# Kernel optimization log

Measured on AMD Instinct MI355X. Metric: run time of the kernel, lower is better.

The kernel has to match this reference:

```python
import jax, jax.numpy as jnp
import numpy as np

R = 32            # voxel resolution
DIM = 240         # channels C
EPS_NORM = 0.0    # module eps
BN_EPS = 1e-5     # torch BatchNorm1d default eps


def setup_inputs() -> dict:
    key = jax.random.key(0)
    k1, k2, k3 = jax.random.split(key, 3)
    B, C, N = 4, DIM, 32768
    features = jax.random.normal(k1, (B, C, N), jnp.float32)
    coords = jax.random.uniform(k2, (B, 3, N), jnp.float32)
    # mlp params: Conv1d(2C -> C, kernel 1) + BatchNorm1d(C)
    w = jax.random.normal(k3, (C, 2 * C), jnp.float32) / np.sqrt(2 * C).astype(np.float32)
    b = jnp.zeros((C,), jnp.float32)
    gamma = jnp.ones((C,), jnp.float32)
    beta = jnp.zeros((C,), jnp.float32)
    return {"features": features, "coords": coords, "w": w, "b": b, "gamma": gamma, "beta": beta}


def _voxelize(features, coords):
    # normalize coords into [0, 1], scale to voxel grid
    nc = coords - coords.mean(axis=2, keepdims=True)                      # [B,3,N]
    scale = jnp.linalg.norm(nc, axis=1, keepdims=True).max(axis=2, keepdims=True) * 2.0 + EPS_NORM
    nc = nc / scale + 0.5
    nc = jnp.clip(nc * R, 0, R - 1)
    vox = jnp.round(nc).astype(jnp.int32)
    pos = vox[:, 0] + vox[:, 1] * R + vox[:, 2] * (R * R)                 # [B,N] flattened voxel id
    R3 = R * R * R

    def per_batch(f, p):
        # f: [C,N], p: [N] -> [2C, R3]; per-voxel max feature + second (min) feature
        mx = jax.ops.segment_max(f.T, p, num_segments=R3)                 # [R3, C]
        mn = jax.ops.segment_min(f.T, p, num_segments=R3)                 # [R3, C]
        cnt = jax.ops.segment_sum(jnp.ones_like(p), p, num_segments=R3)  # [R3]
        mask = (cnt > 0)[:, None]
        mx = jnp.where(mask, mx, 0.0)
        mn = jnp.where(mask, mn, 0.0)
        return jnp.concatenate([mx, mn], axis=1).T                        # [2C, R3]

    fea = jax.vmap(per_batch)(features, pos)                              # [B,2C,R3]
    return fea, nc


def reference(features, coords, w, b, gamma, beta):
    fea, nc = _voxelize(features, coords)
    # 1x1 Conv1d (pointwise GEMM) + BatchNorm1d (training-mode batch stats) + Swish
    y = jnp.einsum('co,bov->bcv', w, fea) + b[None, :, None]
    mean = y.mean(axis=(0, 2), keepdims=True)
    var = y.var(axis=(0, 2), keepdims=True)
    y = gamma[None, :, None] * (y - mean) * jax.lax.rsqrt(var + BN_EPS) + beta[None, :, None]
    y = y * jax.nn.sigmoid(y)
    B, C, _ = features.shape
    return y.reshape(B, C, R, R, R), nc
```

## Files before the change

kernel.cpp:

```cpp
#include <hip/hip_runtime.h>
#include <cstdint>
#include <cstddef>

#define RR 32
#define R3 32768
#define NPT 32768
#define CH 240
#define CH2 480
#define NB 4
#define NTILES 2048
#define Y_ELEMS 31457280

typedef __attribute__((ext_vector_type(8))) short short8v;
typedef __attribute__((ext_vector_type(4))) short short4v;
typedef __attribute__((ext_vector_type(4))) float float4v;

union u8pack { short8v v; unsigned short u[8]; };
union u4pack { short4v v; unsigned short u[4]; };

static __device__ __forceinline__ float bf2f(unsigned short u) {
  return __uint_as_float(((unsigned int)u) << 16);
}
static __device__ __forceinline__ unsigned short f2bf(float f) {
  unsigned int u = __float_as_uint(f);
  u = (u + 0x7FFFu + ((u >> 16) & 1u)) >> 16;
  return (unsigned short)u;
}

__global__ void k_init(int* __restrict__ cnt, float* __restrict__ stats,
                       const float* __restrict__ w, unsigned short* __restrict__ wfrag,
                       int* __restrict__ tilectr) {
  int g = blockIdx.x * 256 + threadIdx.x;
  if (g == 0) *tilectr = 0;
  if (g < NB * R3) cnt[g] = 0;
  if (g < 4096) stats[g] = 0.0f;
  if (g < 14400) {
    int lane = g & 63, t = g >> 6;
    int mg = t / 75, r = t % 75;
    int kc = r / 5, mL = r % 5;
    int m = mg * 5 + mL;
    int ln = lane & 15, q = lane >> 4;
    const float* src = w + (size_t)(m * 16 + ln) * CH2 + kc * 32 + q * 8;
    u8pack pk;
#pragma unroll
    for (int j = 0; j < 8; j++) pk.u[j] = f2bf(src[j]);
    *(short8v*)&wfrag[(size_t)g * 8] = pk.v;
  }
}

__global__ __launch_bounds__(1024) void k_coord_stats(const float* __restrict__ coords,
                                                      float* __restrict__ ms) {
  __shared__ float red[1024];
  __shared__ float mean[3];
  int b = blockIdx.x, t = threadIdx.x;
  const float4* cb4 = (const float4*)(coords + (size_t)b * 3 * NPT);
  float s[3] = {0.f, 0.f, 0.f};
  for (int i = t; i < NPT / 4; i += 1024) {
#pragma unroll
    for (int d = 0; d < 3; d++) {
      float4 v = cb4[d * (NPT / 4) + i];
      s[d] += (v.x + v.y) + (v.z + v.w);
    }
  }
  for (int d = 0; d < 3; d++) {
    red[t] = s[d]; __syncthreads();
    for (int k = 512; k > 0; k >>= 1) { if (t < k) red[t] += red[t + k]; __syncthreads(); }
    if (t == 0) mean[d] = red[0] * (1.0f / NPT);
    __syncthreads();
  }
  float m0 = mean[0], m1 = mean[1], m2 = mean[2];
  float mx = 0.f;
  for (int i = t; i < NPT / 4; i += 1024) {
    float4 x = cb4[i], y = cb4[NPT / 4 + i], z = cb4[2 * (NPT / 4) + i];
    float dx, dy, dz, n;
    dx = x.x - m0; dy = y.x - m1; dz = z.x - m2; n = dx * dx + dy * dy + dz * dz; mx = fmaxf(mx, n);
    dx = x.y - m0; dy = y.y - m1; dz = z.y - m2; n = dx * dx + dy * dy + dz * dz; mx = fmaxf(mx, n);
    dx = x.z - m0; dy = y.z - m1; dz = z.z - m2; n = dx * dx + dy * dy + dz * dz; mx = fmaxf(mx, n);
    dx = x.w - m0; dy = y.w - m1; dz = z.w - m2; n = dx * dx + dy * dy + dz * dz; mx = fmaxf(mx, n);
  }
  red[t] = mx; __syncthreads();
  for (int k = 512; k > 0; k >>= 1) { if (t < k) red[t] = fmaxf(red[t], red[t + k]); __syncthreads(); }
  if (t == 0) {
    ms[b * 4 + 0] = m0; ms[b * 4 + 1] = m1; ms[b * 4 + 2] = m2;
    ms[b * 4 + 3] = sqrtf(red[0]) * 2.0f;
  }
}

__global__ void k_pos_nc(const float* __restrict__ coords, const float* __restrict__ ms,
                         float* __restrict__ ncout, int* __restrict__ pos, int* __restrict__ cnt) {
  int g = blockIdx.x * 256 + threadIdx.x;
  int b = g >> 15, i = g & (NPT - 1);
  const float* cb = coords + (size_t)b * 3 * NPT;
  float scale = ms[b * 4 + 3];
  int vox[3];
#pragma unroll
  for (int d = 0; d < 3; d++) {
    float v = (cb[(size_t)d * NPT + i] - ms[b * 4 + d]) / scale + 0.5f;
    v = fminf(fmaxf(v * (float)RR, 0.0f), (float)(RR - 1));
    ncout[((size_t)(b * 3 + d)) * NPT + i] = v;
    vox[d] = (int)rintf(v);
  }
  int p = (b << 15) | (vox[0] + (vox[1] << 5) + (vox[2] << 10));
  pos[g] = p;
  atomicAdd(&cnt[p], 1);
}

__global__ void k_scan(const int* __restrict__ cnt, int* __restrict__ offs) {
  __shared__ int part[1024];
  int b = blockIdx.x, t = threadIdx.x;
  const int base = b * R3;
  int local[32];
  int s = 0;
#pragma unroll
  for (int j = 0; j < 32; j++) { local[j] = cnt[base + t * 32 + j]; s += local[j]; }
  part[t] = s; __syncthreads();
  for (int d = 1; d < 1024; d <<= 1) {
    int v = (t >= d) ? part[t - d] : 0;
    __syncthreads();
    part[t] += v;
    __syncthreads();
  }
  int run = (t == 0) ? 0 : part[t - 1];
#pragma unroll
  for (int j = 0; j < 32; j++) { offs[base + t * 32 + j] = run; run += local[j]; }
}

__global__ void k_scatter(const int* __restrict__ pos, int* __restrict__ offs,
                          int* __restrict__ rank) {
  int g = blockIdx.x * 256 + threadIdx.x;
  int p = pos[g];
  int slot = atomicAdd(&offs[p], 1);
  rank[g] = slot;
}

__global__ __launch_bounds__(256, 4) void k_transpose3(const float* __restrict__ f,
                                                       const int* __restrict__ rank,
                                                       unsigned short* __restrict__ fts) {
  __shared__ unsigned short tile[CH * 68];
  __shared__ int slts[64];
  int p0 = blockIdx.x * 64, b = blockIdx.y;
  int t = threadIdx.x;
  if (t < 64) slts[t] = rank[b * NPT + p0 + t];
  {
    int pg = t & 15, cq = t >> 4;
    const float* src = f + ((size_t)b * CH + cq) * NPT + p0 + pg * 4;
#pragma unroll
    for (int j = 0; j < 15; ++j) {
      float4 v = *(const float4*)(src + (size_t)(j * 16) * NPT);
      int c = j * 16 + cq;
      u4pack p4;
      p4.u[0] = f2bf(v.x); p4.u[1] = f2bf(v.y); p4.u[2] = f2bf(v.z); p4.u[3] = f2bf(v.w);
      *(short4v*)&tile[c * 68 + pg * 4] = p4.v;
    }
  }
  __syncthreads();
  int ch8 = t & 7;
#pragma unroll
  for (int pass = 0; pass < 2; ++pass) {
    int p = pass * 32 + (t >> 3);
    unsigned short* dst = fts + ((size_t)(b * NPT + slts[p])) * CH;
#pragma unroll
    for (int i = 0; i < 4; ++i) {
      int ch = ch8 + 8 * i;
      if (ch < 30) {
        u8pack pk;
#pragma unroll
        for (int jj = 0; jj < 8; ++jj) pk.u[jj] = tile[(ch * 8 + jj) * 68 + p];
        *(short8v*)&dst[ch * 8] = pk.v;
      }
    }
  }
}

__global__ __launch_bounds__(512, 2) void k_fused(const int* __restrict__ cnt,
                                                  const int* __restrict__ offs,
                                                  const unsigned short* __restrict__ fts,
                                                  const unsigned short* __restrict__ wfrag,
                                                  const float* __restrict__ bias,
                                                  unsigned short* __restrict__ ybf,
                                                  float* __restrict__ gstats,
                                                  int* __restrict__ tilectr) {
  __shared__ unsigned short fB[2][4 * 15 * 512];
  __shared__ int scnt[2][64], soffs[2][64], vlist[2][64], elist[2][64];
  __shared__ int qh[2], qm[2], em[2], tq[4];
  int tid = threadIdx.x;
  int wave = tid >> 6, lane = tid & 63;
  int sub = lane >> 5, l = lane & 31;
  int ln = lane & 15, q = lane >> 4;

  int nmt = (wave == 7) ? 1 : 2;
  short8v wreg[2][15];
#pragma unroll
  for (int mm = 0; mm < 2; ++mm)
    if (mm < nmt) {
      int mt = wave * 2 + mm;
      int mg = mt / 5, mL = mt % 5;
      const unsigned short* wp = wfrag + ((size_t)(mg * 75 + mL) * 512) + lane * 8;
#pragma unroll
      for (int kc = 0; kc < 15; ++kc)
        wreg[mm][kc] = *(const short8v*)(wp + (size_t)kc * 5 * 512);
    }

  float bb[2][4];
#pragma unroll
  for (int mm = 0; mm < 2; ++mm)
    if (mm < nmt) {
      int mt = wave * 2 + mm;
#pragma unroll
      for (int r = 0; r < 4; ++r) bb[mm][r] = bias[mt * 16 + q * 4 + r];
    }
  float sacc[2][4], sqacc[2][4];
#pragma unroll
  for (int mm = 0; mm < 2; ++mm)
#pragma unroll
    for (int r = 0; r < 4; ++r) { sacc[mm][r] = 0.f; sqacc[mm][r] = 0.f; }

  int t1c = 30 + l;
  int kc0 = l >> 2, q0 = l & 3;
  int kc1 = t1c >> 2, q1 = t1c & 3;
  int proc = wave * 2 + sub;

  auto BUILD = [&](int sb, int n, int off) {
    scnt[sb][lane] = n; soffs[sb][lane] = off;
    unsigned long long m = __ballot(n > 0);
    int pfx = __popcll(m & ((1ull << lane) - 1ull));
    if (n > 0) vlist[sb][pfx] = lane;
    int epfx = lane - pfx;
    if (n == 0) elist[sb][epfx] = lane;
    if (lane == 0) { qm[sb] = __popcll(m); em[sb] = 64 - __popcll(m); qh[sb] = 0; }
  };

  auto GATHER = [&](int sb, int T) {
    unsigned short* fb = fB[sb];
    int bbase = (T >> 9) << 15;
    int qmL = qm[sb];
    while (true) {
      int p;
      if (l == 0) p = atomicAdd(&qh[sb], 1);
      p = __shfl(p, sub << 5);
      if (p >= qmL) break;
      int lv = vlist[sb][p];
      int n = scnt[sb][lv];
      int start = soffs[sb][lv] - n;
      int cg = lv >> 4, cc = lv & 15;
      if (l < 30) {
        const unsigned short* sp = fts + (size_t)(bbase + start) * CH + l * 8;
        int lim = (n - 1) * CH;
        float mx[8], mn[8];
#pragma unroll
        for (int k = 0; k < 8; k++) { mx[k] = -__builtin_inff(); mn[k] = __builtin_inff(); }
        for (int j = 0; j < n; j += 8) {
          int base = j * CH;
          u8pack u0, u1, u2, u3, u4, u5, u6, u7;
          int o0 = base;           o0 = o0 < lim ? o0 : lim;
          int o1 = base + CH;      o1 = o1 < lim ? o1 : lim;
          int o2 = base + 2 * CH;  o2 = o2 < lim ? o2 : lim;
          int o3 = base + 3 * CH;  o3 = o3 < lim ? o3 : lim;
          int o4 = base + 4 * CH;  o4 = o4 < lim ? o4 : lim;
          int o5 = base + 5 * CH;  o5 = o5 < lim ? o5 : lim;
          int o6 = base + 6 * CH;  o6 = o6 < lim ? o6 : lim;
          int o7 = base + 7 * CH;  o7 = o7 < lim ? o7 : lim;
          u0.v = *(const short8v*)(sp + o0);
          u1.v = *(const short8v*)(sp + o1);
          u2.v = *(const short8v*)(sp + o2);
          u3.v = *(const short8v*)(sp + o3);
          u4.v = *(const short8v*)(sp + o4);
          u5.v = *(const short8v*)(sp + o5);
          u6.v = *(const short8v*)(sp + o6);
          u7.v = *(const short8v*)(sp + o7);
#pragma unroll
          for (int k = 0; k < 8; k++) {
            float a0 = bf2f(u0.u[k]), a1 = bf2f(u1.u[k]);
            float a2 = bf2f(u2.u[k]), a3 = bf2f(u3.u[k]);
            float a4 = bf2f(u4.u[k]), a5 = bf2f(u5.u[k]);
            float a6 = bf2f(u6.u[k]), a7 = bf2f(u7.u[k]);
            float hx = fmaxf(fmaxf(fmaxf(a0, a1), fmaxf(a2, a3)),
                             fmaxf(fmaxf(a4, a5), fmaxf(a6, a7)));
            float hn = fminf(fminf(fminf(a0, a1), fminf(a2, a3)),
                             fminf(fminf(a4, a5), fminf(a6, a7)));
            mx[k] = fmaxf(mx[k], hx);
            mn[k] = fminf(mn[k], hn);
          }
        }
        u8pack omx, omn;
#pragma unroll
        for (int k = 0; k < 8; k++) { omx.u[k] = f2bf(mx[k]); omn.u[k] = f2bf(mn[k]); }
        int ci0 = (q0 * 16 + cc) ^ (kc0 & 7);
        int ci1 = (q1 * 16 + cc) ^ (kc1 & 7);
        *(short8v*)&fb[((cg * 15 + kc0) * 64 + ci0) * 8] = omx.v;
        *(short8v*)&fb[((cg * 15 + kc1) * 64 + ci1) * 8] = omn.v;
      }
    }
    int emL = em[sb];
    if (l < 30) {
      u8pack z;
#pragma unroll
      for (int k = 0; k < 8; k++) z.u[k] = 0;
      for (int e = proc; e < emL; e += 16) {
        int lv = elist[sb][e];
        int cg = lv >> 4, cc = lv & 15;
        int ci0 = (q0 * 16 + cc) ^ (kc0 & 7);
        int ci1 = (q1 * 16 + cc) ^ (kc1 & 7);
        *(short8v*)&fb[((cg * 15 + kc0) * 64 + ci0) * 8] = z.v;
        *(short8v*)&fb[((cg * 15 + kc1) * 64 + ci1) * 8] = z.v;
      }
    }
  };

  if (wave == 0) {
    int t;
    if (lane == 0) t = atomicAdd(tilectr, 1);
    int T0w = __shfl(t, 0);
    if (lane == 0) t = atomicAdd(tilectr, 1);
    int T1w = __shfl(t, 0);
    if (lane == 0) { tq[0] = T0w; tq[1] = T1w; }
    int na = 0, oa = 0, nb2 = 0, ob = 0;
    if (T0w < NTILES) { na = cnt[T0w * 64 + lane]; oa = offs[T0w * 64 + lane]; }
    if (T1w < NTILES) { nb2 = cnt[T1w * 64 + lane]; ob = offs[T1w * 64 + lane]; }
    BUILD(0, na, oa);
    BUILD(1, nb2, ob);
  }
  __syncthreads();
  {
    int T0v = tq[0];
    if (T0v < NTILES) GATHER(0, T0v);
  }

  for (int it = 0;; ++it) {
    __syncthreads();
    int T = tq[it & 3];
    if (T >= NTILES) break;
    int cb = it & 1, nb = cb ^ 1;
    int Tn = tq[(it + 1) & 3];

    int n2 = 0, o2 = 0;
    if (wave == 0) {
      int t;
      if (lane == 0) t = atomicAdd(tilectr, 1);
      int Tn2 = __shfl(t, 0);
      if (lane == 0) tq[(it + 2) & 3] = Tn2;
      if (Tn2 < NTILES) { n2 = cnt[Tn2 * 64 + lane]; o2 = offs[Tn2 * 64 + lane]; }
    }
    __syncthreads();

    if (Tn < NTILES) GATHER(nb, Tn);

    float4v acc[2][4];
#pragma unroll
    for (int mm = 0; mm < 2; ++mm)
#pragma unroll
      for (int cg = 0; cg < 4; ++cg) acc[mm][cg] = (float4v){0.f, 0.f, 0.f, 0.f};

    const unsigned short* fbase = fB[cb];
#pragma unroll
    for (int kc = 0; kc < 15; ++kc) {
      const unsigned short* fbl = fbase + (size_t)((lane ^ (kc & 7)) * 8);
      short8v bfv[4];
#pragma unroll
      for (int cg = 0; cg < 4; ++cg)
        bfv[cg] = *(const short8v*)(fbl + (size_t)(cg * 15 + kc) * 512);
#pragma unroll
      for (int mm = 0; mm < 2; ++mm)
        if (mm < nmt)
#pragma unroll
          for (int cg = 0; cg < 4; ++cg)
            acc[mm][cg] = __builtin_amdgcn_mfma_f32_16x16x32_bf16(wreg[mm][kc], bfv[cg], acc[mm][cg], 0, 0, 0);
    }

    int bt = T >> 9;
    int v0 = (T & 511) * 64;
    unsigned short* yb = ybf + ((size_t)bt * CH) * R3 + v0 + ln;
#pragma unroll
    for (int mm = 0; mm < 2; ++mm)
      if (mm < nmt) {
        int mt = wave * 2 + mm;
#pragma unroll
        for (int r = 0; r < 4; ++r) {
          int c = mt * 16 + q * 4 + r;
          unsigned short* yrow = yb + (size_t)c * R3;
          float bbv = bb[mm][r];
          float s = 0.f, sq = 0.f;
#pragma unroll
          for (int cg = 0; cg < 4; ++cg) {
            float yv = acc[mm][cg][r] + bbv;
            yrow[cg * 16] = f2bf(yv);
            s += yv; sq += yv * yv;
          }
          sacc[mm][r] += s;
          sqacc[mm][r] += sq;
        }
      }

    if (wave == 0) BUILD(it & 1, n2, o2);
  }

  float* gslot = gstats + (size_t)(blockIdx.x & 7) * 512;
#pragma unroll
  for (int mm = 0; mm < 2; ++mm)
    if (mm < nmt) {
      int mt = wave * 2 + mm;
#pragma unroll
      for (int r = 0; r < 4; ++r) {
        float s = sacc[mm][r], sq = sqacc[mm][r];
#pragma unroll
        for (int off = 1; off < 16; off <<= 1) {
          s += __shfl_xor(s, off);
          sq += __shfl_xor(sq, off);
        }
        if (ln == 0) {
          int c = mt * 16 + q * 4 + r;
          atomicAdd(&gslot[c], s);
          atomicAdd(&gslot[256 + c], sq);
        }
      }
    }
}

__global__ void k_bnpre(const float* __restrict__ stats, const float* __restrict__ gamma,
                        const float* __restrict__ beta, float* __restrict__ bnsh) {
  int c = threadIdx.x;
  if (c < CH) {
    const float ninv = 1.0f / (float)(NB * R3);
    float sum = 0.f, ssq = 0.f;
#pragma unroll
    for (int sl = 0; sl < 8; ++sl) {
      sum += stats[sl * 512 + c];
      ssq += stats[sl * 512 + 256 + c];
    }
    float mean = sum * ninv;
    float var = ssq * ninv - mean * mean;
    float s = gamma[c] * rsqrtf(var + 1e-5f);
    bnsh[c] = s;
    bnsh[CH + c] = beta[c] - mean * s;
  }
}

__global__ void k_apply(const unsigned short* __restrict__ ybf, float* __restrict__ out,
                        const float* __restrict__ bnsh) {
  int g = blockIdx.x * 256 + threadIdx.x;
  int c = (g >> 12) % CH;
  float s = bnsh[c];
  float h = bnsh[CH + c];
  u8pack v;
  v.v = *(const short8v*)(ybf + (size_t)g * 8);
  float4 o0, o1;
  float t;
  t = bf2f(v.u[0]) * s + h; o0.x = t / (1.0f + __expf(-t));
  t = bf2f(v.u[1]) * s + h; o0.y = t / (1.0f + __expf(-t));
  t = bf2f(v.u[2]) * s + h; o0.z = t / (1.0f + __expf(-t));
  t = bf2f(v.u[3]) * s + h; o0.w = t / (1.0f + __expf(-t));
  t = bf2f(v.u[4]) * s + h; o1.x = t / (1.0f + __expf(-t));
  t = bf2f(v.u[5]) * s + h; o1.y = t / (1.0f + __expf(-t));
  t = bf2f(v.u[6]) * s + h; o1.z = t / (1.0f + __expf(-t));
  t = bf2f(v.u[7]) * s + h; o1.w = t / (1.0f + __expf(-t));
  ((float4*)out)[(size_t)g * 2] = o0;
  ((float4*)out)[(size_t)g * 2 + 1] = o1;
}

extern "C" void kernel_launch(void* const* d_in, const int* in_sizes, int n_in,
                              void* d_out, int out_size, void* d_ws, size_t ws_size,
                              hipStream_t stream) {
  const float* features = (const float*)d_in[0];
  const float* coords   = (const float*)d_in[1];
  const float* w        = (const float*)d_in[2];
  const float* bias     = (const float*)d_in[3];
  const float* gamma    = (const float*)d_in[4];
  const float* beta     = (const float*)d_in[5];
  float* out = (float*)d_out;

  char* ws = (char*)d_ws;
  size_t off = 0;
  float* ms    = (float*)(ws + off); off += 256;
  int* tilectr = (int*)(ws + off);   off += 256;
  float* stats = (float*)(ws + off); off += 16384;
  float* bnsh  = (float*)(ws + off); off += 2048;
  int* pos     = (int*)(ws + off);   off += (size_t)NB * NPT * 4;
  int* cnt     = (int*)(ws + off);   off += (size_t)NB * R3 * 4;
  int* offs    = (int*)(ws + off);   off += (size_t)NB * R3 * 4;
  int* rank    = (int*)(ws + off);   off += (size_t)NB * NPT * 4;
  unsigned short* wfrag = (unsigned short*)(ws + off); off += (size_t)CH * CH2 * 2;
  unsigned short* fts   = (unsigned short*)(ws + off); off += (size_t)NB * NPT * CH * 2;
  unsigned short* ybf   = (unsigned short*)(ws + off); off += (size_t)NB * R3 * CH * 2;

  float* ncout = out + Y_ELEMS;

  k_init<<<516, 256, 0, stream>>>(cnt, stats, w, wfrag, tilectr);
  k_coord_stats<<<4, 1024, 0, stream>>>(coords, ms);
  k_pos_nc<<<512, 256, 0, stream>>>(coords, ms, ncout, pos, cnt);
  k_scan<<<4, 1024, 0, stream>>>(cnt, offs);
  k_scatter<<<512, 256, 0, stream>>>(pos, offs, rank);
  k_transpose3<<<dim3(512, 4), 256, 0, stream>>>(features, rank, fts);
  k_fused<<<256, 512, 0, stream>>>(cnt, offs, fts, wfrag, bias, ybf, stats, tilectr);
  k_bnpre<<<1, 256, 0, stream>>>(stats, gamma, beta, bnsh);
  k_apply<<<Y_ELEMS / 2048, 256, 0, stream>>>(ybf, out, bnsh);
}
```

Before: 369.6 us.

## Fuse init, scatter and BN-finalize kernels and widen apply per thread

Merges the coordinate-statistics kernel into the init kernel. Folds the per-point atomic slot assignment into the transpose kernel, which removes the rank buffer. Computes the BatchNorm scale and shift in the last-finishing block of the fused GEMM kernel, using a second atomic counter. Also pairs two points per thread in the transpose writeback and doubles the work per thread in the apply kernel. The aim is to cut three kernel launches and one intermediate buffer round-trip. The cost is a last-block pattern with a threadfence and atomic reads, plus less parallelism in apply.

New measurement: 417.7 us. 1.13x slower.

```diff
diff --git a/kernel.cpp b/kernel.cpp
--- a/kernel.cpp
+++ b/kernel.cpp
@@ -27,31 +27,33 @@
   return (unsigned short)u;
 }
 
-__global__ void k_init(int* __restrict__ cnt, float* __restrict__ stats,
-                       const float* __restrict__ w, unsigned short* __restrict__ wfrag,
-                       int* __restrict__ tilectr) {
-  int g = blockIdx.x * 256 + threadIdx.x;
-  if (g == 0) *tilectr = 0;
-  if (g < NB * R3) cnt[g] = 0;
-  if (g < 4096) stats[g] = 0.0f;
-  if (g < 14400) {
-    int lane = g & 63, t = g >> 6;
-    int mg = t / 75, r = t % 75;
-    int kc = r / 5, mL = r % 5;
-    int m = mg * 5 + mL;
-    int ln = lane & 15, q = lane >> 4;
-    const float* src = w + (size_t)(m * 16 + ln) * CH2 + kc * 32 + q * 8;
-    u8pack pk;
-#pragma unroll
-    for (int j = 0; j < 8; j++) pk.u[j] = f2bf(src[j]);
-    *(short8v*)&wfrag[(size_t)g * 8] = pk.v;
-  }
-}
-
-__global__ __launch_bounds__(1024) void k_coord_stats(const float* __restrict__ coords,
-                                                      float* __restrict__ ms) {
+__global__ __launch_bounds__(1024) void k_init(const float* __restrict__ coords,
+                                               float* __restrict__ ms,
+                                               int* __restrict__ cnt, float* __restrict__ stats,
+                                               const float* __restrict__ w,
+                                               unsigned short* __restrict__ wfrag,
+                                               int* __restrict__ ctrs) {
   __shared__ float red[1024];
   __shared__ float mean[3];
+  if (blockIdx.x >= 4) {
+    int g = (blockIdx.x - 4) * 1024 + threadIdx.x;
+    if (g < 2) ctrs[g] = 0;
+    if (g < NB * R3) cnt[g] = 0;
+    if (g < 4096) stats[g] = 0.0f;
+    if (g < 14400) {
+      int lane = g & 63, t = g >> 6;
+      int mg = t / 75, r = t % 75;
+      int kc = r / 5, mL = r % 5;
+      int m = mg * 5 + mL;
+      int ln = lane & 15, q = lane >> 4;
+      const float* src = w + (size_t)(m * 16 + ln) * CH2 + kc * 32 + q * 8;
+      u8pack pk;
+#pragma unroll
+      for (int j = 0; j < 8; j++) pk.u[j] = f2bf(src[j]);
+      *(short8v*)&wfrag[(size_t)g * 8] = pk.v;
+    }
+    return;
+  }
   int b = blockIdx.x, t = threadIdx.x;
   const float4* cb4 = (const float4*)(coords + (size_t)b * 3 * NPT);
   float s[3] = {0.f, 0.f, 0.f};
@@ -125,22 +127,18 @@
   for (int j = 0; j < 32; j++) { offs[base + t * 32 + j] = run; run += local[j]; }
 }
 
-__global__ void k_scatter(const int* __restrict__ pos, int* __restrict__ offs,
-                          int* __restrict__ rank) {
-  int g = blockIdx.x * 256 + threadIdx.x;
-  int p = pos[g];
-  int slot = atomicAdd(&offs[p], 1);
-  rank[g] = slot;
-}
-
 __global__ __launch_bounds__(256, 4) void k_transpose3(const float* __restrict__ f,
-                                                       const int* __restrict__ rank,
+                                                       const int* __restrict__ pos,
+                                                       int* __restrict__ offs,
                                                        unsigned short* __restrict__ fts) {
   __shared__ unsigned short tile[CH * 68];
   __shared__ int slts[64];
   int p0 = blockIdx.x * 64, b = blockIdx.y;
   int t = threadIdx.x;
-  if (t < 64) slts[t] = rank[b * NPT + p0 + t];
+  if (t < 64) {
+    int p = pos[b * NPT + p0 + t];
+    slts[t] = atomicAdd(&offs[p], 1);
+  }
   {
     int pg = t & 15, cq = t >> 4;
     const float* src = f + ((size_t)b * CH + cq) * NPT + p0 + pg * 4;
@@ -155,19 +153,22 @@
   }
   __syncthreads();
   int ch8 = t & 7;
-#pragma unroll
-  for (int pass = 0; pass < 2; ++pass) {
-    int p = pass * 32 + (t >> 3);
-    unsigned short* dst = fts + ((size_t)(b * NPT + slts[p])) * CH;
-#pragma unroll
-    for (int i = 0; i < 4; ++i) {
-      int ch = ch8 + 8 * i;
-      if (ch < 30) {
-        u8pack pk;
-#pragma unroll
-        for (int jj = 0; jj < 8; ++jj) pk.u[jj] = tile[(ch * 8 + jj) * 68 + p];
-        *(short8v*)&dst[ch * 8] = pk.v;
+  int pr = t >> 3;
+  unsigned short* dstA = fts + ((size_t)(b * NPT + slts[2 * pr])) * CH;
+  unsigned short* dstB = fts + ((size_t)(b * NPT + slts[2 * pr + 1])) * CH;
+#pragma unroll
+  for (int i = 0; i < 4; ++i) {
+    int ch = ch8 + 8 * i;
+    if (ch < 30) {
+      u8pack pkA, pkB;
+#pragma unroll
+      for (int jj = 0; jj < 8; ++jj) {
+        unsigned int v = *(const unsigned int*)&tile[(ch * 8 + jj) * 68 + 2 * pr];
+        pkA.u[jj] = (unsigned short)(v & 0xffffu);
+        pkB.u[jj] = (unsigned short)(v >> 16);
       }
+      *(short8v*)&dstA[ch * 8] = pkA.v;
+      *(short8v*)&dstB[ch * 8] = pkB.v;
     }
   }
 }
@@ -179,10 +180,14 @@
                                                   const float* __restrict__ bias,
                                                   unsigned short* __restrict__ ybf,
                                                   float* __restrict__ gstats,
-                                                  int* __restrict__ tilectr) {
+                                                  int* __restrict__ ctrs,
+                                                  const float* __restrict__ gamma,
+                                                  const float* __restrict__ beta,
+                                                  float* __restrict__ bnsh) {
   __shared__ unsigned short fB[2][4 * 15 * 512];
   __shared__ int scnt[2][64], soffs[2][64], vlist[2][64], elist[2][64];
   __shared__ int qh[2], qm[2], em[2], tq[4];
+  __shared__ int lastflag;
   int tid = threadIdx.x;
   int wave = tid >> 6, lane = tid & 63;
   int sub = lane >> 5, l = lane & 31;
@@ -309,9 +314,9 @@
 
   if (wave == 0) {
     int t;
-    if (lane == 0) t = atomicAdd(tilectr, 1);
+    if (lane == 0) t = atomicAdd(&ctrs[0], 1);
     int T0w = __shfl(t, 0);
-    if (lane == 0) t = atomicAdd(tilectr, 1);
+    if (lane == 0) t = atomicAdd(&ctrs[0], 1);
     int T1w = __shfl(t, 0);
     if (lane == 0) { tq[0] = T0w; tq[1] = T1w; }
     int na = 0, oa = 0, nb2 = 0, ob = 0;
@@ -336,7 +341,7 @@
     int n2 = 0, o2 = 0;
     if (wave == 0) {
       int t;
-      if (lane == 0) t = atomicAdd(tilectr, 1);
+      if (lane == 0) t = atomicAdd(&ctrs[0], 1);
       int Tn2 = __shfl(t, 0);
       if (lane == 0) tq[(it + 2) & 3] = Tn2;
       if (Tn2 < NTILES) { n2 = cnt[Tn2 * 64 + lane]; o2 = offs[Tn2 * 64 + lane]; }
@@ -414,47 +419,58 @@
         }
       }
     }
-}
-
-__global__ void k_bnpre(const float* __restrict__ stats, const float* __restrict__ gamma,
-                        const float* __restrict__ beta, float* __restrict__ bnsh) {
-  int c = threadIdx.x;
-  if (c < CH) {
+
+  __threadfence();
+  if (tid == 0) lastflag = (atomicAdd(&ctrs[1], 1) == (int)gridDim.x - 1);
+  __syncthreads();
+  if (lastflag && tid < CH) {
     const float ninv = 1.0f / (float)(NB * R3);
     float sum = 0.f, ssq = 0.f;
 #pragma unroll
     for (int sl = 0; sl < 8; ++sl) {
-      sum += stats[sl * 512 + c];
-      ssq += stats[sl * 512 + 256 + c];
+      sum += atomicAdd(&gstats[sl * 512 + tid], 0.0f);
+      ssq += atomicAdd(&gstats[sl * 512 + 256 + tid], 0.0f);
     }
     float mean = sum * ninv;
     float var = ssq * ninv - mean * mean;
-    float s = gamma[c] * rsqrtf(var + 1e-5f);
-    bnsh[c] = s;
-    bnsh[CH + c] = beta[c] - mean * s;
+    float s = gamma[tid] * rsqrtf(var + 1e-5f);
+    bnsh[tid] = s;
+    bnsh[CH + tid] = beta[tid] - mean * s;
   }
 }
 
 __global__ void k_apply(const unsigned short* __restrict__ ybf, float* __restrict__ out,
                         const float* __restrict__ bnsh) {
-  int g = blockIdx.x * 256 + threadIdx.x;
+  int g2 = blockIdx.x * 256 + threadIdx.x;
+  int g = g2 * 2;
   int c = (g >> 12) % CH;
   float s = bnsh[c];
   float h = bnsh[CH + c];
-  u8pack v;
-  v.v = *(const short8v*)(ybf + (size_t)g * 8);
-  float4 o0, o1;
+  u8pack va, vb;
+  va.v = *(const short8v*)(ybf + (size_t)g * 8);
+  vb.v = *(const short8v*)(ybf + (size_t)(g + 1) * 8);
+  float4 o0, o1, o2, o3;
   float t;
-  t = bf2f(v.u[0]) * s + h; o0.x = t / (1.0f + __expf(-t));
-  t = bf2f(v.u[1]) * s + h; o0.y = t / (1.0f + __expf(-t));
-  t = bf2f(v.u[2]) * s + h; o0.z = t / (1.0f + __expf(-t));
-  t = bf2f(v.u[3]) * s + h; o0.w = t / (1.0f + __expf(-t));
-  t = bf2f(v.u[4]) * s + h; o1.x = t / (1.0f + __expf(-t));
-  t = bf2f(v.u[5]) * s + h; o1.y = t / (1.0f + __expf(-t));
-  t = bf2f(v.u[6]) * s + h; o1.z = t / (1.0f + __expf(-t));
-  t = bf2f(v.u[7]) * s + h; o1.w = t / (1.0f + __expf(-t));
-  ((float4*)out)[(size_t)g * 2] = o0;
+  t = bf2f(va.u[0]) * s + h; o0.x = t / (1.0f + __expf(-t));
+  t = bf2f(va.u[1]) * s + h; o0.y = t / (1.0f + __expf(-t));
+  t = bf2f(va.u[2]) * s + h; o0.z = t / (1.0f + __expf(-t));
+  t = bf2f(va.u[3]) * s + h; o0.w = t / (1.0f + __expf(-t));
+  t = bf2f(va.u[4]) * s + h; o1.x = t / (1.0f + __expf(-t));
+  t = bf2f(va.u[5]) * s + h; o1.y = t / (1.0f + __expf(-t));
+  t = bf2f(va.u[6]) * s + h; o1.z = t / (1.0f + __expf(-t));
+  t = bf2f(va.u[7]) * s + h; o1.w = t / (1.0f + __expf(-t));
+  t = bf2f(vb.u[0]) * s + h; o2.x = t / (1.0f + __expf(-t));
+  t = bf2f(vb.u[1]) * s + h; o2.y = t / (1.0f + __expf(-t));
+  t = bf2f(vb.u[2]) * s + h; o2.z = t / (1.0f + __expf(-t));
+  t = bf2f(vb.u[3]) * s + h; o2.w = t / (1.0f + __expf(-t));
+  t = bf2f(vb.u[4]) * s + h; o3.x = t / (1.0f + __expf(-t));
+  t = bf2f(vb.u[5]) * s + h; o3.y = t / (1.0f + __expf(-t));
+  t = bf2f(vb.u[6]) * s + h; o3.z = t / (1.0f + __expf(-t));
+  t = bf2f(vb.u[7]) * s + h; o3.w = t / (1.0f + __expf(-t));
+  ((float4*)out)[(size_t)g * 2]     = o0;
   ((float4*)out)[(size_t)g * 2 + 1] = o1;
+  ((float4*)out)[(size_t)g * 2 + 2] = o2;
+  ((float4*)out)[(size_t)g * 2 + 3] = o3;
 }
 
 extern "C" void kernel_launch(void* const* d_in, const int* in_sizes, int n_in,
@@ -471,26 +487,22 @@
   char* ws = (char*)d_ws;
   size_t off = 0;
   float* ms    = (float*)(ws + off); off += 256;
-  int* tilectr = (int*)(ws + off);   off += 256;
+  int* ctrs    = (int*)(ws + off);   off += 256;
   float* stats = (float*)(ws + off); off += 16384;
   float* bnsh  = (float*)(ws + off); off += 2048;
   int* pos     = (int*)(ws + off);   off += (size_t)NB * NPT * 4;
   int* cnt     = (int*)(ws + off);   off += (size_t)NB * R3 * 4;
   int* offs    = (int*)(ws + off);   off += (size_t)NB * R3 * 4;
-  int* rank    = (int*)(ws + off);   off += (size_t)NB * NPT * 4;
   unsigned short* wfrag = (unsigned short*)(ws + off); off += (size_t)CH * CH2 * 2;
   unsigned short* fts   = (unsigned short*)(ws + off); off += (size_t)NB * NPT * CH * 2;
   unsigned short* ybf   = (unsigned short*)(ws + off); off += (size_t)NB * R3 * CH * 2;
 
   float* ncout = out + Y_ELEMS;
 
-  k_init<<<516, 256, 0, stream>>>(cnt, stats, w, wfrag, tilectr);
-  k_coord_stats<<<4, 1024, 0, stream>>>(coords, ms);
+  k_init<<<133, 1024, 0, stream>>>(coords, ms, cnt, stats, w, wfrag, ctrs);
   k_pos_nc<<<512, 256, 0, stream>>>(coords, ms, ncout, pos, cnt);
   k_scan<<<4, 1024, 0, stream>>>(cnt, offs);
-  k_scatter<<<512, 256, 0, stream>>>(pos, offs, rank);
-  k_transpose3<<<dim3(512, 4), 256, 0, stream>>>(features, rank, fts);
-  k_fused<<<256, 512, 0, stream>>>(cnt, offs, fts, wfrag, bias, ybf, stats, tilectr);
-  k_bnpre<<<1, 256, 0, stream>>>(stats, gamma, beta, bnsh);
-  k_apply<<<Y_ELEMS / 2048, 256, 0, stream>>>(ybf, out, bnsh);
-}
+  k_transpose3<<<dim3(512, 4), 256, 0, stream>>>(features, pos, offs, fts);
+  k_fused<<<256, 512, 0, stream>>>(cnt, offs, fts, wfrag, bias, ybf, stats, ctrs, gamma, beta, bnsh);
+  k_apply<<<Y_ELEMS / 4096, 256, 0, stream>>>(ybf, out, bnsh);
+}
```
